# Kernel optimization log

Measured on AMD Instinct MI355X. Metric: run time of the kernel, lower is better.

Reference implementation:

```python
import jax, jax.numpy as jnp
import numpy as np

# Module config (matches init_kwargs shape_data=[8,32,32], pow=1, spde_type='adv_diff')
N_T, N_Y, N_X = 8, 32, 32
N = N_Y * N_X            # nb_nodes
DX = DY = DT = 1.0


def build_A(kappa, m1, m2, h11, h12, h22):
    """Dense [N,N] advection-diffusion operator A = kappa^2 I + m.grad - div(H grad),
    central differences on the n_y x n_x grid, zero-Dirichlet boundary (9-pt stencil).
    All coefficient inputs are [N] vectors (node-wise)."""
    ii, jj = jnp.divmod(jnp.arange(N), N_X)   # ii: y index, jj: x index
    rows = jnp.arange(N)
    A = jnp.zeros((N, N), dtype=kappa.dtype)
    # center
    A = A.at[rows, rows].add(kappa ** 2 + 2.0 * h11 / DX**2 + 2.0 * h22 / DY**2)

    def add(A, di, dj, coef):
        vi, vj = ii + di, jj + dj
        valid = (vi >= 0) & (vi < N_Y) & (vj >= 0) & (vj < N_X)
        cols = jnp.clip(vi, 0, N_Y - 1) * N_X + jnp.clip(vj, 0, N_X - 1)
        return A.at[rows, cols].add(jnp.where(valid, coef, 0.0))

    A = add(A, 0, +1, -h11 / DX**2 + m1 / (2.0 * DX))
    A = add(A, 0, -1, -h11 / DX**2 - m1 / (2.0 * DX))
    A = add(A, +1, 0, -h22 / DY**2 + m2 / (2.0 * DY))
    A = add(A, -1, 0, -h22 / DY**2 - m2 / (2.0 * DY))
    cxy = h12 / (2.0 * DX * DY)    # cross term -2*H12*u_xy with /(4 dx dy) stencil
    A = add(A, +1, +1, -cxy)
    A = add(A, -1, -1, -cxy)
    A = add(A, +1, -1, +cxy)
    A = add(A, -1, +1, +cxy)
    return A


def _forward(kappa, m, H, tau):
    n_b = kappa.shape[0]
    # reorder field params to [n_b, n_t, N]
    kap = jnp.moveaxis(kappa[:, 0], -1, 1)
    m1 = jnp.moveaxis(m[:, 0], -1, 1)
    m2 = jnp.moveaxis(m[:, 1], -1, 1)
    h11 = jnp.moveaxis(H[:, 0, 0], -1, 1)
    h12 = jnp.moveaxis(H[:, 0, 1], -1, 1)
    h22 = jnp.moveaxis(H[:, 1, 1], -1, 1)
    tau_ = jnp.moveaxis(tau[:, 0], -1, 1)

    flat = lambda a: a.reshape(n_b * N_T, N)
    A = jax.vmap(build_A)(flat(kap), flat(m1), flat(m2), flat(h11), flat(h12), flat(h22))
    A = A.reshape(n_b, N_T, N, N)                 # B = A since pow == 1

    eye = jnp.eye(N, dtype=A.dtype)
    M = eye + DT * A                               # inv_M_k = I + dt*B_k, [n_b,n_t,N,N]
    w = DT / (tau_ ** 2)                           # Qs_tilde_k = diag(dt / tau_k^2)

    WM = w[..., :, None] * M                       # diag(w_k) @ M_k
    P = jnp.einsum('btij,btik->btjk', M, WM)       # M_k^T diag(w_k) M_k

    # diagonal blocks: D_k = P_k + diag(w_{k+1}) for k < n_t-1; D_{n_t-1} = P_{n_t-1}
    w_next = jnp.concatenate([w[:, 1:], jnp.zeros_like(w[:, :1])], axis=1)
    D = P + w_next[..., :, None] * eye

    # sub-diagonal block (k, k-1) = -M_k^T diag(w_k), k = 1..n_t-1 (0-block padded at front)
    zblk = jnp.zeros((n_b, 1, N, N), dtype=A.dtype)
    lower = jnp.concatenate([zblk, -jnp.swapaxes(WM[:, 1:], -1, -2)], axis=1)
    # super-diagonal block (k, k+1) = -diag(w_{k+1}) M_{k+1}, k = 0..n_t-2 (0-block at end)
    upper = jnp.concatenate([-WM[:, 1:], zblk], axis=1)

    # block-tridiagonal precision Q, packed as [n_b, 3(diag,lower,upper), n_t, N, N]
    return jnp.stack([D, lower, upper], axis=1)


def setup_inputs() -> dict:
    key = jax.random.key(0)
    ks = jax.random.split(key, 4)
    n_b = 2
    kappa = 0.1 + 0.9 * jax.random.uniform(ks[0], (n_b, 1, N, N_T), dtype=jnp.float32)
    m = 0.2 * jax.random.normal(ks[1], (n_b, 2, N, N_T), dtype=jnp.float32)
    H = jax.random.uniform(ks[2], (n_b, 2, 2, N, N_T), dtype=jnp.float32)
    H = H.at[:, 0, 1].multiply(0.2)
    H = H.at[:, 1, 0].set(H[:, 0, 1])              # symmetric diffusion tensor
    tau = 0.5 + jax.random.uniform(ks[3], (n_b, 1, N, N_T), dtype=jnp.float32)
    return {"kappa": kappa, "m": m, "H": H, "tau": tau}


def reference(kappa, m, H, tau):
    return _forward(kappa, m, H, tau)
```

## Files before the change

kernel.cpp:

```cpp
#include <hip/hip_runtime.h>

#define NT 8
#define NY 32
#define NX 32
#define NN 1024

__device__ __forceinline__ void node_coefs(const float* __restrict__ kap,
                                           const float* __restrict__ m,
                                           const float* __restrict__ H,
                                           const float* __restrict__ tau,
                                           int b, int node, int tc,
                                           int iy, int ix,
                                           float* c , float& w) {
    const int base = node * NT + tc;
    const float kp  = kap[(b * NN) * NT + base];
    const float m1  = m[((b * 2 + 0) * NN) * NT + base];
    const float m2  = m[((b * 2 + 1) * NN) * NT + base];
    const float h11 = H[((b * 4 + 0) * NN) * NT + base];
    const float h12 = H[((b * 4 + 1) * NN) * NT + base];
    const float h22 = H[((b * 4 + 3) * NN) * NT + base];
    const float tv  = tau[(b * NN) * NT + base];
    w = 1.0f / (tv * tv);

    const float cxy = 0.5f * h12;
    const bool ym = (iy - 1) >= 0, yp = (iy + 1) < NY;
    const bool xm = (ix - 1) >= 0, xp = (ix + 1) < NX;

    c[4] = 1.0f + kp * kp + 2.0f * h11 + 2.0f * h22;
    c[0] = (ym && xm) ? -cxy               : 0.0f;
    c[1] =  ym        ? (-h22 - 0.5f * m2) : 0.0f;
    c[2] = (ym && xp) ?  cxy               : 0.0f;
    c[3] =  xm        ? (-h11 - 0.5f * m1) : 0.0f;
    c[5] =  xp        ? (-h11 + 0.5f * m1) : 0.0f;
    c[6] = (yp && xm) ?  cxy               : 0.0f;
    c[7] =  yp        ? (-h22 + 0.5f * m2) : 0.0f;
    c[8] = (yp && xp) ? -cxy               : 0.0f;
}

__global__ __launch_bounds__(256) void spde_kernel(const float* __restrict__ kap,
                                                   const float* __restrict__ m,
                                                   const float* __restrict__ H,
                                                   const float* __restrict__ tau,
                                                   float* __restrict__ out) {
    __shared__ float sc[9][9];
    __shared__ float sw[9];
    __shared__ float vals[25];

    const int row = blockIdx.x;
    const int j   = row & (NN - 1);
    const int t   = (row >> 10) & 7;
    const int bb  = row >> 13;
    const int blk = bb % 3;
    const int b   = bb / 3;
    const int jy = j >> 5, jx = j & 31;
    const int tid = threadIdx.x;

    const bool zero_row = (blk == 1 && t == 0) || (blk == 2 && t == NT - 1);

    if (!zero_row) {
        const int tc = (blk == 2) ? t + 1 : t;

        if (tid < 9) {
            const int ey = tid / 3 - 1, ex = tid % 3 - 1;
            const int iy = jy + ey, ix = jx + ex;
            float c[9];
            float w = 0.0f;
            if (iy >= 0 && iy < NY && ix >= 0 && ix < NX) {
                node_coefs(kap, m, H, tau, b, iy * NX + ix, tc, iy, ix, c, w);
            } else {
                #pragma unroll
                for (int q = 0; q < 9; ++q) c[q] = 0.0f;
            }
            #pragma unroll
            for (int q = 0; q < 9; ++q) sc[tid][q] = c[q];
            sw[tid] = w;
        }
        __syncthreads();

        if (blk == 0) {
            if (tid < 25) {
                const int dy = tid / 5 - 2, dx = tid % 5 - 2;
                float acc = 0.0f;
                #pragma unroll
                for (int d = 0; d < 9; ++d) {
                    const int ey = d / 3 - 1, ex = d % 3 - 1;
                    const int r2y = dy - ey, r2x = dx - ex;
                    if (r2y >= -1 && r2y <= 1 && r2x >= -1 && r2x <= 1) {
                        acc += sw[d] * sc[d][8 - d] * sc[d][(r2y + 1) * 3 + (r2x + 1)];
                    }
                }
                if (tid == 12 && t < NT - 1) {
                    const float tv = tau[(size_t)(b * NN + j) * NT + (t + 1)];
                    acc += 1.0f / (tv * tv);
                }
                vals[tid] = acc;
            }
        } else if (blk == 1) {
            if (tid < 9) {
                vals[tid] = -sw[tid] * sc[tid][8 - tid];
            }
        } else {
            if (tid < 9) {
                vals[tid] = -sw[4] * sc[4][tid];
            }
        }
        __syncthreads();
    }

    float4 v = make_float4(0.f, 0.f, 0.f, 0.f);
    if (!zero_row) {
        const int R = (blk == 0) ? 2 : 1;
        const int W = 2 * R + 1;
        const int c0 = tid * 4;
        float* vp = &v.x;
        #pragma unroll
        for (int q = 0; q < 4; ++q) {
            const int c = c0 + q;
            const int cy = c >> 5, cx = c & 31;
            const int ddy = cy - jy, ddx = cx - jx;
            if (ddy >= -R && ddy <= R && ddx >= -R && ddx <= R) {
                v = v;
                vp[q] = vals[(ddy + R) * W + (ddx + R)];
            }
        }
    }
    float4* op = (float4*)(out + (size_t)row * NN);
    op[tid] = v;
}

extern "C" void kernel_launch(void* const* d_in, const int* in_sizes, int n_in,
                              void* d_out, int out_size, void* d_ws, size_t ws_size,
                              hipStream_t stream) {
    const float* kap = (const float*)d_in[0];
    const float* m   = (const float*)d_in[1];
    const float* H   = (const float*)d_in[2];
    const float* tau = (const float*)d_in[3];
    float* out = (float*)d_out;

    const int n_b = in_sizes[0] / (NN * NT);
    const int grid = n_b * 3 * NT * NN;
    spde_kernel<<<grid, 256, 0, stream>>>(kap, m, H, tau, out);
}
```

Before: 200.1 us.

## Split into coefficient precompute kernel and streaming writer kernel

Before, every output row's block recomputed its 9 neighbor node coefficients and stencil products through shared memory with two barriers. Now a precompute kernel (one block per batch/time, 1024 threads) computes each node's scaled coefficients U and 25-entry diagonal-block stencil D0 once into workspace. A barrier-free writer kernel then streams the dense output, gathering the few nonzeros from those tables. This removes redundant per-row work and synchronization. In exchange it adds a second launch and a global workspace round-trip, and uses about 40KB of shared memory in the precompute block.

Result: slower. 212.3 us (+6.1%).

```diff
diff --git a/kernel.cpp b/kernel.cpp
--- a/kernel.cpp
+++ b/kernel.cpp
@@ -23,8 +23,8 @@
     w = 1.0f / (tv * tv);
 
     const float cxy = 0.5f * h12;
-    const bool ym = (iy - 1) >= 0, yp = (iy + 1) < NY;
-    const bool xm = (ix - 1) >= 0, xp = (ix + 1) < NX;
+    const bool ym = iy > 0, yp = iy < NY - 1;
+    const bool xm = ix > 0, xp = ix < NX - 1;
 
     c[4] = 1.0f + kp * kp + 2.0f * h11 + 2.0f * h22;
     c[0] = (ym && xm) ? -cxy               : 0.0f;
@@ -37,95 +37,115 @@
     c[8] = (yp && xp) ? -cxy               : 0.0f;
 }
 
-__global__ __launch_bounds__(256) void spde_kernel(const float* __restrict__ kap,
-                                                   const float* __restrict__ m,
-                                                   const float* __restrict__ H,
-                                                   const float* __restrict__ tau,
-                                                   float* __restrict__ out) {
-    __shared__ float sc[9][9];
-    __shared__ float sw[9];
-    __shared__ float vals[25];
+__global__ __launch_bounds__(1024) void precompute_kernel(
+        const float* __restrict__ kap, const float* __restrict__ m,
+        const float* __restrict__ H, const float* __restrict__ tau,
+        float* __restrict__ U, float* __restrict__ D0) {
+    __shared__ float sc[NN][9];
+    __shared__ float sw[NN];
 
-    const int row = blockIdx.x;
+    const int bt = blockIdx.x;
+    const int b = bt >> 3, t = bt & 7;
+    const int j = threadIdx.x;
+    const int jy = j >> 5, jx = j & 31;
+
+    float c[9], w;
+    node_coefs(kap, m, H, tau, b, j, t, jy, jx, c, w);
+
+    {
+        float* up = U + ((size_t)bt * NN + j) * 9;
+        #pragma unroll
+        for (int q = 0; q < 9; ++q) up[q] = -w * c[q];
+    }
+    #pragma unroll
+    for (int q = 0; q < 9; ++q) sc[j][q] = c[q];
+    sw[j] = w;
+    __syncthreads();
+
+    float wnext = 0.0f;
+    if (t < NT - 1) {
+        const float tv = tau[((size_t)b * NN + j) * NT + (t + 1)];
+        wnext = 1.0f / (tv * tv);
+    }
+
+    float* dp = D0 + ((size_t)bt * NN + j) * 25;
+    #pragma unroll
+    for (int dy = -2; dy <= 2; ++dy) {
+        #pragma unroll
+        for (int dx = -2; dx <= 2; ++dx) {
+            float acc = 0.0f;
+            #pragma unroll
+            for (int d = 0; d < 9; ++d) {
+                const int ey = d / 3 - 1, ex = d % 3 - 1;
+                const int r2y = dy - ey, r2x = dx - ex;
+                if (r2y < -1 || r2y > 1 || r2x < -1 || r2x > 1) continue;
+                const int iy = jy + ey, ix = jx + ex;
+                if (iy < 0 || iy >= NY || ix < 0 || ix >= NX) continue;
+                const int jn = iy * NX + ix;
+                acc += sw[jn] * sc[jn][8 - d] * sc[jn][(r2y + 1) * 3 + (r2x + 1)];
+            }
+            if (dy == 0 && dx == 0) acc += wnext;
+            dp[(dy + 2) * 5 + (dx + 2)] = acc;
+        }
+    }
+}
+
+__global__ __launch_bounds__(256) void writer_kernel(
+        const float* __restrict__ U, const float* __restrict__ D0,
+        float* __restrict__ out) {
+    const unsigned gid = blockIdx.x * 256u + threadIdx.x;
+    const unsigned row = gid >> 8;
+    const unsigned q   = gid & 255u;
+
     const int j   = row & (NN - 1);
     const int t   = (row >> 10) & 7;
     const int bb  = row >> 13;
     const int blk = bb % 3;
     const int b   = bb / 3;
     const int jy = j >> 5, jx = j & 31;
-    const int tid = threadIdx.x;
+    const int cy = q >> 3;
+    const int cx0 = (q & 7) * 4;
 
-    const bool zero_row = (blk == 1 && t == 0) || (blk == 2 && t == NT - 1);
+    float4 v = make_float4(0.f, 0.f, 0.f, 0.f);
+    float* vp = &v.x;
+    const int ddy = cy - jy;
 
-    if (!zero_row) {
-        const int tc = (blk == 2) ? t + 1 : t;
-
-        if (tid < 9) {
-            const int ey = tid / 3 - 1, ex = tid % 3 - 1;
-            const int iy = jy + ey, ix = jx + ex;
-            float c[9];
-            float w = 0.0f;
-            if (iy >= 0 && iy < NY && ix >= 0 && ix < NX) {
-                node_coefs(kap, m, H, tau, b, iy * NX + ix, tc, iy, ix, c, w);
-            } else {
-                #pragma unroll
-                for (int q = 0; q < 9; ++q) c[q] = 0.0f;
-            }
+    if (blk == 0) {
+        if (ddy >= -2 && ddy <= 2) {
+            const float* base = D0 + ((size_t)(b * NT + t) * NN + j) * 25
+                                   + (ddy + 2) * 5;
             #pragma unroll
-            for (int q = 0; q < 9; ++q) sc[tid][q] = c[q];
-            sw[tid] = w;
-        }
-        __syncthreads();
-
-        if (blk == 0) {
-            if (tid < 25) {
-                const int dy = tid / 5 - 2, dx = tid % 5 - 2;
-                float acc = 0.0f;
-                #pragma unroll
-                for (int d = 0; d < 9; ++d) {
-                    const int ey = d / 3 - 1, ex = d % 3 - 1;
-                    const int r2y = dy - ey, r2x = dx - ex;
-                    if (r2y >= -1 && r2y <= 1 && r2x >= -1 && r2x <= 1) {
-                        acc += sw[d] * sc[d][8 - d] * sc[d][(r2y + 1) * 3 + (r2x + 1)];
-                    }
-                }
-                if (tid == 12 && t < NT - 1) {
-                    const float tv = tau[(size_t)(b * NN + j) * NT + (t + 1)];
-                    acc += 1.0f / (tv * tv);
-                }
-                vals[tid] = acc;
-            }
-        } else if (blk == 1) {
-            if (tid < 9) {
-                vals[tid] = -sw[tid] * sc[tid][8 - tid];
-            }
-        } else {
-            if (tid < 9) {
-                vals[tid] = -sw[4] * sc[4][tid];
+            for (int qq = 0; qq < 4; ++qq) {
+                const int ddx = cx0 + qq - jx;
+                if (ddx >= -2 && ddx <= 2) vp[qq] = base[ddx + 2];
             }
         }
-        __syncthreads();
-    }
-
-    float4 v = make_float4(0.f, 0.f, 0.f, 0.f);
-    if (!zero_row) {
-        const int R = (blk == 0) ? 2 : 1;
-        const int W = 2 * R + 1;
-        const int c0 = tid * 4;
-        float* vp = &v.x;
-        #pragma unroll
-        for (int q = 0; q < 4; ++q) {
-            const int c = c0 + q;
-            const int cy = c >> 5, cx = c & 31;
-            const int ddy = cy - jy, ddx = cx - jx;
-            if (ddy >= -R && ddy <= R && ddx >= -R && ddx <= R) {
-                v = v;
-                vp[q] = vals[(ddy + R) * W + (ddx + R)];
+    } else if (blk == 1) {
+        if (t > 0 && ddy >= -1 && ddy <= 1) {
+            #pragma unroll
+            for (int qq = 0; qq < 4; ++qq) {
+                const int ddx = cx0 + qq - jx;
+                if (ddx >= -1 && ddx <= 1) {
+                    const int k = (cy * NX) + (cx0 + qq);
+                    const int off = (ddy + 1) * 3 + (ddx + 1);
+                    vp[qq] = U[((size_t)(b * NT + t) * NN + k) * 9 + (8 - off)];
+                }
+            }
+        }
+    } else {
+        if (t < NT - 1 && ddy >= -1 && ddy <= 1) {
+            const float* up = U + ((size_t)(b * NT + t + 1) * NN + j) * 9
+                                + (ddy + 1) * 3;
+            #pragma unroll
+            for (int qq = 0; qq < 4; ++qq) {
+                const int ddx = cx0 + qq - jx;
+                if (ddx >= -1 && ddx <= 1) vp[qq] = up[ddx + 1];
             }
         }
     }
-    float4* op = (float4*)(out + (size_t)row * NN);
-    op[tid] = v;
+
+    float4* op = (float4*)out;
+    op[gid] = v;
 }
 
 extern "C" void kernel_launch(void* const* d_in, const int* in_sizes, int n_in,
@@ -138,6 +158,12 @@
     float* out = (float*)d_out;
 
     const int n_b = in_sizes[0] / (NN * NT);
-    const int grid = n_b * 3 * NT * NN;
-    spde_kernel<<<grid, 256, 0, stream>>>(kap, m, H, tau, out);
+
+    float* U  = (float*)d_ws;
+    float* D0 = U + (size_t)n_b * NT * NN * 9;
+
+    precompute_kernel<<<n_b * NT, 1024, 0, stream>>>(kap, m, H, tau, U, D0);
+
+    const unsigned total_quads = (unsigned)n_b * 3u * NT * NN * (NN / 4);
+    writer_kernel<<<total_quads / 256u, 256, 0, stream>>>(U, D0, out);
 }
```

## Fuse diagonal, lower and upper block rows into one workgroup per (b,t,j)

Applied to the files above, without the earlier changes.

Each workgroup now handles one (batch, time, node) triple and writes the matching rows of the diagonal, lower and upper blocks, instead of launching one workgroup per row of each block. The stencil coefficients and weights are loaded once and shared by all three outputs, which cuts the grid to a third and removes the repeated coefficient loads. The upper block is written at index t-1, and the last upper block is zero-filled by the t=7 workgroup. Each workgroup does more serial work in exchange, and the index mapping must now be correct for three output matrices at once.

After: 199.3 us. About the same (-0.4%).

```diff
diff --git a/kernel.cpp b/kernel.cpp
--- a/kernel.cpp
+++ b/kernel.cpp
@@ -23,8 +23,8 @@
     w = 1.0f / (tv * tv);
 
     const float cxy = 0.5f * h12;
-    const bool ym = (iy - 1) >= 0, yp = (iy + 1) < NY;
-    const bool xm = (ix - 1) >= 0, xp = (ix + 1) < NX;
+    const bool ym = iy > 0, yp = iy < NY - 1;
+    const bool xm = ix > 0, xp = ix < NX - 1;
 
     c[4] = 1.0f + kp * kp + 2.0f * h11 + 2.0f * h22;
     c[0] = (ym && xm) ? -cxy               : 0.0f;
@@ -44,88 +44,112 @@
                                                    float* __restrict__ out) {
     __shared__ float sc[9][9];
     __shared__ float sw[9];
-    __shared__ float vals[25];
+    __shared__ float valsD[25];
+    __shared__ float valsL[9];
+    __shared__ float valsU[9];
 
-    const int row = blockIdx.x;
-    const int j   = row & (NN - 1);
-    const int t   = (row >> 10) & 7;
-    const int bb  = row >> 13;
-    const int blk = bb % 3;
-    const int b   = bb / 3;
+    const int gb = blockIdx.x;
+    const int j  = gb & (NN - 1);
+    const int bt = gb >> 10;
+    const int t  = bt & 7;
+    const int b  = bt >> 3;
     const int jy = j >> 5, jx = j & 31;
     const int tid = threadIdx.x;
 
-    const bool zero_row = (blk == 1 && t == 0) || (blk == 2 && t == NT - 1);
+    if (tid < 9) {
+        const int ey = tid / 3 - 1, ex = tid % 3 - 1;
+        const int iy = jy + ey, ix = jx + ex;
+        float c[9];
+        float w = 0.0f;
+        if (iy >= 0 && iy < NY && ix >= 0 && ix < NX) {
+            node_coefs(kap, m, H, tau, b, iy * NX + ix, t, iy, ix, c, w);
+        } else {
+            #pragma unroll
+            for (int q = 0; q < 9; ++q) c[q] = 0.0f;
+        }
+        #pragma unroll
+        for (int q = 0; q < 9; ++q) sc[tid][q] = c[q];
+        sw[tid] = w;
+    }
+    __syncthreads();
 
-    if (!zero_row) {
-        const int tc = (blk == 2) ? t + 1 : t;
-
-        if (tid < 9) {
-            const int ey = tid / 3 - 1, ex = tid % 3 - 1;
-            const int iy = jy + ey, ix = jx + ex;
-            float c[9];
-            float w = 0.0f;
-            if (iy >= 0 && iy < NY && ix >= 0 && ix < NX) {
-                node_coefs(kap, m, H, tau, b, iy * NX + ix, tc, iy, ix, c, w);
-            } else {
-                #pragma unroll
-                for (int q = 0; q < 9; ++q) c[q] = 0.0f;
-            }
-            #pragma unroll
-            for (int q = 0; q < 9; ++q) sc[tid][q] = c[q];
-            sw[tid] = w;
-        }
-        __syncthreads();
-
-        if (blk == 0) {
-            if (tid < 25) {
-                const int dy = tid / 5 - 2, dx = tid % 5 - 2;
-                float acc = 0.0f;
-                #pragma unroll
-                for (int d = 0; d < 9; ++d) {
-                    const int ey = d / 3 - 1, ex = d % 3 - 1;
-                    const int r2y = dy - ey, r2x = dx - ex;
-                    if (r2y >= -1 && r2y <= 1 && r2x >= -1 && r2x <= 1) {
-                        acc += sw[d] * sc[d][8 - d] * sc[d][(r2y + 1) * 3 + (r2x + 1)];
-                    }
-                }
-                if (tid == 12 && t < NT - 1) {
-                    const float tv = tau[(size_t)(b * NN + j) * NT + (t + 1)];
-                    acc += 1.0f / (tv * tv);
-                }
-                vals[tid] = acc;
-            }
-        } else if (blk == 1) {
-            if (tid < 9) {
-                vals[tid] = -sw[tid] * sc[tid][8 - tid];
-            }
-        } else {
-            if (tid < 9) {
-                vals[tid] = -sw[4] * sc[4][tid];
+    if (tid < 25) {
+        const int dy = tid / 5 - 2, dx = tid % 5 - 2;
+        float acc = 0.0f;
+        #pragma unroll
+        for (int d = 0; d < 9; ++d) {
+            const int ey = d / 3 - 1, ex = d % 3 - 1;
+            const int r2y = dy - ey, r2x = dx - ex;
+            if (r2y >= -1 && r2y <= 1 && r2x >= -1 && r2x <= 1) {
+                acc += sw[d] * sc[d][8 - d] * sc[d][(r2y + 1) * 3 + (r2x + 1)];
             }
         }
-        __syncthreads();
+        if (tid == 12 && t < NT - 1) {
+            const float tv = tau[((size_t)b * NN + j) * NT + (t + 1)];
+            acc += 1.0f / (tv * tv);
+        }
+        valsD[tid] = acc;
+    } else if (tid >= 64 && tid < 73) {
+        const int d = tid - 64;
+        valsL[d] = -sw[d] * sc[d][8 - d];
+    } else if (tid >= 73 && tid < 82) {
+        const int q = tid - 73;
+        valsU[q] = -sw[4] * sc[4][q];
     }
+    __syncthreads();
 
-    float4 v = make_float4(0.f, 0.f, 0.f, 0.f);
-    if (!zero_row) {
-        const int R = (blk == 0) ? 2 : 1;
-        const int W = 2 * R + 1;
-        const int c0 = tid * 4;
-        float* vp = &v.x;
-        #pragma unroll
-        for (int q = 0; q < 4; ++q) {
-            const int c = c0 + q;
-            const int cy = c >> 5, cx = c & 31;
-            const int ddy = cy - jy, ddx = cx - jx;
-            if (ddy >= -R && ddy <= R && ddx >= -R && ddx <= R) {
-                v = v;
-                vp[q] = vals[(ddy + R) * W + (ddx + R)];
+    const int cy  = tid >> 3;
+    const int cx0 = (tid & 7) * 4;
+    const int ddy = cy - jy;
+    float4* const outq = (float4*)out;
+    const size_t rowq = ((size_t)j << 8) + tid;
+    const size_t matD = ((size_t)(b * 3 + 0) * NT + t) << 18;
+    const size_t matL = ((size_t)(b * 3 + 1) * NT + t) << 18;
+
+    {
+        float4 v = make_float4(0.f, 0.f, 0.f, 0.f);
+        if (ddy >= -2 && ddy <= 2) {
+            float* vp = &v.x;
+            const float* wrow = &valsD[(ddy + 2) * 5 + 2];
+            #pragma unroll
+            for (int qq = 0; qq < 4; ++qq) {
+                const int ddx = cx0 + qq - jx;
+                if (ddx >= -2 && ddx <= 2) vp[qq] = wrow[ddx];
             }
         }
+        outq[matD + rowq] = v;
     }
-    float4* op = (float4*)(out + (size_t)row * NN);
-    op[tid] = v;
+    {
+        float4 v = make_float4(0.f, 0.f, 0.f, 0.f);
+        if (t > 0 && ddy >= -1 && ddy <= 1) {
+            float* vp = &v.x;
+            const float* wrow = &valsL[(ddy + 1) * 3 + 1];
+            #pragma unroll
+            for (int qq = 0; qq < 4; ++qq) {
+                const int ddx = cx0 + qq - jx;
+                if (ddx >= -1 && ddx <= 1) vp[qq] = wrow[ddx];
+            }
+        }
+        outq[matL + rowq] = v;
+    }
+    if (t >= 1) {
+        const size_t matU = ((size_t)(b * 3 + 2) * NT + (t - 1)) << 18;
+        float4 v = make_float4(0.f, 0.f, 0.f, 0.f);
+        if (ddy >= -1 && ddy <= 1) {
+            float* vp = &v.x;
+            const float* wrow = &valsU[(ddy + 1) * 3 + 1];
+            #pragma unroll
+            for (int qq = 0; qq < 4; ++qq) {
+                const int ddx = cx0 + qq - jx;
+                if (ddx >= -1 && ddx <= 1) vp[qq] = wrow[ddx];
+            }
+        }
+        outq[matU + rowq] = v;
+        if (t == NT - 1) {
+            const size_t matU7 = ((size_t)(b * 3 + 2) * NT + 7) << 18;
+            outq[matU7 + rowq] = make_float4(0.f, 0.f, 0.f, 0.f);
+        }
+    }
 }
 
 extern "C" void kernel_launch(void* const* d_in, const int* in_sizes, int n_in,
@@ -138,6 +162,6 @@
     float* out = (float*)d_out;
 
     const int n_b = in_sizes[0] / (NN * NT);
-    const int grid = n_b * 3 * NT * NN;
+    const int grid = n_b * NT * NN;
     spde_kernel<<<grid, 256, 0, stream>>>(kap, m, H, tau, out);
 }
```
